# Kernel optimization log

Measured on AMD Instinct MI355X. Metric: run time of the kernel, lower is better.

Reference implementation:

```python
import jax, jax.numpy as jnp
import numpy as np

CHANNELS = 512
COND_DIM = 768
NUM_HEADS = 8
NUM_GROUPS = 32
EPS = 1e-5


def setup_inputs() -> dict:
    key = jax.random.key(0)
    ks = jax.random.split(key, 8)
    B, H, W, C, S = 8, 64, 64, CHANNELS, 256
    x = jax.random.normal(ks[0], (B, H, W, C), dtype=jnp.float32)
    cond_tokens = jax.random.normal(ks[1], (B, S, COND_DIM), dtype=jnp.float32)
    gn_scale = jnp.ones((C,), dtype=jnp.float32)
    gn_bias = jnp.zeros((C,), dtype=jnp.float32)
    Wq = jax.random.normal(ks[2], (C, CHANNELS), dtype=jnp.float32) * 0.02
    Wk = jax.random.normal(ks[3], (COND_DIM, CHANNELS), dtype=jnp.float32) * 0.02
    Wv = jax.random.normal(ks[4], (COND_DIM, CHANNELS), dtype=jnp.float32) * 0.02
    Wo = jax.random.normal(ks[5], (CHANNELS, CHANNELS), dtype=jnp.float32) * 0.02
    bo = jnp.zeros((CHANNELS,), dtype=jnp.float32)
    return {"x": x, "cond_tokens": cond_tokens, "gn_scale": gn_scale,
            "gn_bias": gn_bias, "Wq": Wq, "Wk": Wk, "Wv": Wv, "Wo": Wo, "bo": bo}


def group_norm(x, scale, bias):
    # x: (B,H,W,C); normalize over H,W and channels within each of NUM_GROUPS groups
    b, h, w, c = x.shape
    xg = x.reshape(b, h, w, NUM_GROUPS, c // NUM_GROUPS)
    mean = jnp.mean(xg, axis=(1, 2, 4), keepdims=True)
    var = jnp.var(xg, axis=(1, 2, 4), keepdims=True)
    xn = (xg - mean) * jax.lax.rsqrt(var + EPS)
    return xn.reshape(b, h, w, c) * scale + bias


def reference(x, cond_tokens, gn_scale, gn_bias, Wq, Wk, Wv, Wo, bo):
    b, h, w, c = x.shape
    head_dim = CHANNELS // NUM_HEADS
    x_seq = group_norm(x, gn_scale, gn_bias).reshape(b, h * w, c)
    # projections
    q = (x_seq @ Wq).reshape(b, -1, NUM_HEADS, head_dim).transpose(0, 2, 1, 3)
    k = (cond_tokens @ Wk).reshape(b, -1, NUM_HEADS, head_dim).transpose(0, 2, 1, 3)
    v = (cond_tokens @ Wv).reshape(b, -1, NUM_HEADS, head_dim).transpose(0, 2, 1, 3)
    scores = jnp.einsum('bhqd,bhkd->bhqk', q, k) / np.sqrt(head_dim).astype(np.float32)
    attn = jax.nn.softmax(scores, axis=-1)
    out = jnp.einsum('bhqk,bhkd->bhqd', attn, v)
    out = out.transpose(0, 2, 1, 3).reshape(b, h * w, CHANNELS)
    out = out @ Wo + bo
    return x + out.reshape(b, h, w, c)
```

## Files before the change

### kernel.cpp

```cpp
#include <hip/hip_runtime.h>
#include <hip/hip_bf16.h>

typedef unsigned short u16;
typedef unsigned int u32;
typedef __attribute__((ext_vector_type(8))) __bf16 bf16x8;
typedef __attribute__((ext_vector_type(4))) float f32x4;
typedef __attribute__((ext_vector_type(16))) float f32x16;
typedef __attribute__((ext_vector_type(4))) u32 u32x4;

#define DEVFN static __device__ __forceinline__

DEVFN float bf2f(u16 v) { union { u32 u; float f; } x; x.u = (u32)v << 16; return x.f; }
DEVFN u16 f2bf(float f) {
    union { float f; u32 u; } x; x.f = f;
    u32 r = x.u + 0x7fff + ((x.u >> 16) & 1);
    return (u16)(r >> 16);
}

union BF2 { struct { __bf16 lo, hi; } s; u32 w; };
DEVFN u32 pk2(float a, float b) { BF2 t; t.s.lo = (__bf16)a; t.s.hi = (__bf16)b; return t.w; }

DEVFN void gload_lds16(const u16* g, u16* l) {
    __builtin_amdgcn_global_load_lds((const __attribute__((address_space(1))) u32*)g,
                                     (__attribute__((address_space(3))) u32*)l, 16, 0, 0);
}

template<int OUTMODE, bool BIAS, bool RES, bool AFF>
__global__ __launch_bounds__(256)
void gemm_bt(const void* __restrict__ Av, const u16* __restrict__ B,
             const u16* __restrict__ B2,
             void* __restrict__ Cv, void* __restrict__ Cv2,
             const float* __restrict__ bias, const float* __restrict__ res,
             const float* __restrict__ cfA, const float* __restrict__ cfD,
             int K, int lda, int ldb, int ldc, float scale)
{
    __shared__ u16 smem[16384];
    const int tid = threadIdx.x;
    const int lane = tid & 63, wave = tid >> 6;
    const int wr = wave >> 1, wc = wave & 1;
    const u16* Bsel = (OUTMODE == 3 && blockIdx.z) ? B2 : B;
    const u16* Bb = Bsel + (long)blockIdx.y * 128 * ldb;
    const int ra = tid >> 2, ca = (tid & 3) * 8;
    const int foff = ((lane & 15) * 4 + (lane >> 4)) * 8;

    f32x4 acc[4][4];
#pragma unroll
    for (int i = 0; i < 4; ++i)
#pragma unroll
        for (int j = 0; j < 4; ++j) acc[i][j] = (f32x4){0.f, 0.f, 0.f, 0.f};

    const int nt = K >> 5;

    auto stageB = [&](int t, u16* bb) {
#pragma unroll
        for (int p = 0; p < 2; ++p)
            gload_lds16(Bb + (long)(p * 64 + ra) * ldb + t * 32 + ca,
                        bb + (p * 256 + tid) * 8);
    };
    const u16* Ab = (const u16*)Av + (long)blockIdx.x * 128 * lda;
    auto stageA = [&](int t, u16* ab) {
#pragma unroll
        for (int p = 0; p < 2; ++p)
            gload_lds16(Ab + (long)(p * 64 + ra) * lda + t * 32 + ca,
                        ab + (p * 256 + tid) * 8);
    };
    const float* xf = (const float*)Av;
    float4 xr[2][2], ar[2][2], dr[2][2];
    auto affLoad = [&](int t) {
#pragma unroll
        for (int p = 0; p < 2; ++p) {
            long m = (long)blockIdx.x * 128 + p * 64 + ra;
            int c = t * 32 + ca;
            const float* src = xf + m * lda + c;
            xr[p][0] = *(const float4*)(src);
            xr[p][1] = *(const float4*)(src + 4);
            int cb = (int)((m >> 12) << 9) + c;
            ar[p][0] = *(const float4*)(cfA + cb);
            ar[p][1] = *(const float4*)(cfA + cb + 4);
            dr[p][0] = *(const float4*)(cfD + cb);
            dr[p][1] = *(const float4*)(cfD + cb + 4);
        }
    };
    auto affWrite = [&](u16* ab) {
#pragma unroll
        for (int p = 0; p < 2; ++p) {
            u32x4 o;
            o[0] = pk2(xr[p][0].x * ar[p][0].x + dr[p][0].x,
                       xr[p][0].y * ar[p][0].y + dr[p][0].y);
            o[1] = pk2(xr[p][0].z * ar[p][0].z + dr[p][0].z,
                       xr[p][0].w * ar[p][0].w + dr[p][0].w);
            o[2] = pk2(xr[p][1].x * ar[p][1].x + dr[p][1].x,
                       xr[p][1].y * ar[p][1].y + dr[p][1].y);
            o[3] = pk2(xr[p][1].z * ar[p][1].z + dr[p][1].z,
                       xr[p][1].w * ar[p][1].w + dr[p][1].w);
            *(u32x4*)(ab + (p * 256 + tid) * 8) = o;
        }
    };

    stageB(0, smem + 4096);
    if constexpr (AFF) { affLoad(0); affWrite(smem); }
    else               stageA(0, smem);

    int cur = 0;
    for (int t = 0; t < nt; ++t) {
        asm volatile("s_waitcnt vmcnt(0)" ::: "memory");
        __syncthreads();
        const int nxt = cur ^ 1;
        u16* cA = smem + cur * 8192;
        u16* cB = smem + cur * 8192 + 4096;
        u16* nA = smem + nxt * 8192;
        u16* nB = smem + nxt * 8192 + 4096;
        const bool more = (t + 1 < nt);
        if (more) {
            stageB(t + 1, nB);
            if constexpr (AFF) affLoad(t + 1);
            else               stageA(t + 1, nA);
        }
        bf16x8 av[4], bv[4];
#pragma unroll
        for (int i = 0; i < 4; ++i) av[i] = *(const bf16x8*)(cA + (wr * 4 + i) * 512 + foff);
#pragma unroll
        for (int j = 0; j < 4; ++j) bv[j] = *(const bf16x8*)(cB + (wc * 4 + j) * 512 + foff);
        __builtin_amdgcn_s_setprio(1);
#pragma unroll
        for (int i = 0; i < 4; ++i)
#pragma unroll
            for (int j = 0; j < 4; ++j)
                acc[i][j] = __builtin_amdgcn_mfma_f32_16x16x32_bf16(av[i], bv[j], acc[i][j], 0, 0, 0);
        __builtin_amdgcn_s_setprio(0);
        if (more) { if constexpr (AFF) affWrite(nA); }
        cur = nxt;
    }

    const int m0 = blockIdx.x * 128 + wr * 64 + (lane >> 4) * 4;
    const int n0 = blockIdx.y * 128 + wc * 64 + (lane & 15);
    if constexpr (OUTMODE == 0) {
        u16* Cb = (u16*)Cv;
#pragma unroll
        for (int i = 0; i < 4; ++i)
#pragma unroll
            for (int j = 0; j < 4; ++j) {
                int n = n0 + j * 16;
#pragma unroll
                for (int r = 0; r < 4; ++r) {
                    int m = m0 + i * 16 + r;
                    Cb[(long)m * ldc + n] = f2bf(acc[i][j][r] * scale);
                }
            }
    } else if constexpr (OUTMODE == 1) {
        float* cl = (float*)smem;
        float* Co = (float*)Cv;
#pragma unroll
        for (int i = 0; i < 4; ++i) {
            __syncthreads();
#pragma unroll
            for (int j = 0; j < 4; ++j)
#pragma unroll
                for (int r = 0; r < 4; ++r) {
                    int rl = wr * 16 + (lane >> 4) * 4 + r;
                    int col = wc * 64 + j * 16 + (lane & 15);
                    cl[rl * 132 + col] = acc[i][j][r];
                }
            __syncthreads();
            int rl = tid >> 3;
            int c0 = (tid & 7) * 16;
            long m = (long)blockIdx.x * 128 + i * 16 + (rl & 15) + (rl >> 4) * 64;
            long n = (long)blockIdx.y * 128 + c0;
#pragma unroll
            for (int q = 0; q < 4; ++q) {
                float4 v = *(float4*)(cl + rl * 132 + c0 + q * 4);
                float4 o;
                o.x = v.x * scale; o.y = v.y * scale;
                o.z = v.z * scale; o.w = v.w * scale;
                if constexpr (BIAS) {
                    float4 b4 = *(const float4*)(bias + n + q * 4);
                    o.x += b4.x; o.y += b4.y; o.z += b4.z; o.w += b4.w;
                }
                if constexpr (RES) {
                    float4 r4 = *(const float4*)(res + m * ldc + n + q * 4);
                    o.x += r4.x; o.y += r4.y; o.z += r4.z; o.w += r4.w;
                }
                *(float4*)(Co + m * ldc + n + q * 4) = o;
            }
        }
    } else if constexpr (OUTMODE == 2) {
#pragma unroll
        for (int i = 0; i < 4; ++i) {
            int m = m0 + i * 16;
            int b = m >> 8, s = m & 255;
#pragma unroll
            for (int j = 0; j < 4; ++j) {
                int n = n0 + j * 16;
                int h = n >> 6, d = n & 63;
                ushort4 pk;
                pk.x = f2bf(acc[i][j][0]); pk.y = f2bf(acc[i][j][1]);
                pk.z = f2bf(acc[i][j][2]); pk.w = f2bf(acc[i][j][3]);
                *(ushort4*)((u16*)Cv + (((long)(b * 8 + h) * 64 + d) * 256 + s)) = pk;
            }
        }
    } else {
        if (blockIdx.z == 0) {
            u16* Cb = (u16*)Cv;
#pragma unroll
            for (int i = 0; i < 4; ++i)
#pragma unroll
                for (int j = 0; j < 4; ++j) {
                    int n = n0 + j * 16;
#pragma unroll
                    for (int r = 0; r < 4; ++r) {
                        int m = m0 + i * 16 + r;
                        Cb[(long)m * ldc + n] = f2bf(acc[i][j][r] * scale);
                    }
                }
        } else {
#pragma unroll
            for (int i = 0; i < 4; ++i) {
                int m = m0 + i * 16;
                int b = m >> 8, s = m & 255;
#pragma unroll
                for (int j = 0; j < 4; ++j) {
                    int n = n0 + j * 16;
                    int h = n >> 6, d = n & 63;
                    ushort4 pk;
                    pk.x = f2bf(acc[i][j][0]); pk.y = f2bf(acc[i][j][1]);
                    pk.z = f2bf(acc[i][j][2]); pk.w = f2bf(acc[i][j][3]);
                    *(ushort4*)((u16*)Cv2 + (((long)(b * 8 + h) * 64 + d) * 256 + s)) = pk;
                }
            }
        }
    }
}

union U8 { u32 w[4]; bf16x8 v; };

__global__ __launch_bounds__(512, 4)
void attn_fused(const u16* __restrict__ Q, const u16* __restrict__ K,
                const u16* __restrict__ Vt, u16* __restrict__ O)
{
    __shared__ u16 lds[40960];
    const int tid = threadIdx.x, lane = tid & 63, wave = tid >> 6;
    const int bh = blockIdx.y, b = bh >> 3, h = bh & 7;
    const int l31 = lane & 31, lh = lane >> 5;
    const long q0 = (long)b * 4096 + blockIdx.x * 256 + wave * 32;
    const bool hiHalf = (lh != 0);

    {
        const u16* Kb_ = K + (long)b * 256 * 512 + h * 64;
        const u16* Vb_ = Vt + (long)bh * 16384;
#pragma unroll
        for (int it = 0; it < 4; ++it) {
            int f = it * 8 + wave;
            int st = f >> 2, kc = f & 3;
            gload_lds16(Kb_ + (long)(st * 32 + l31) * 512 + kc * 16 + lh * 8,
                        lds + f * 512 + lane * 8);
            int dt = f >> 4, ks = f & 15;
            gload_lds16(Vb_ + (long)(dt * 32 + l31) * 256 + ks * 16 + lh * 8,
                        lds + 16384 + f * 512 + lane * 8);
        }
    }
    bf16x8 qf[4];
    {
        const u16* Qp = Q + (q0 + l31) * 512 + h * 64 + lh * 8;
#pragma unroll
        for (int kc = 0; kc < 4; ++kc) qf[kc] = *(const bf16x8*)(Qp + kc * 16);
    }
    asm volatile("s_waitcnt vmcnt(0)" ::: "memory");
    __syncthreads();

    f32x16 oacc[2];
#pragma unroll
    for (int dt = 0; dt < 2; ++dt)
#pragma unroll
        for (int r = 0; r < 16; ++r) oacc[dt][r] = 0.f;
    float m_run = -3e38f, sum_run = 0.f;

#pragma unroll
    for (int st = 0; st < 8; ++st) {
        f32x16 sc;
#pragma unroll
        for (int r = 0; r < 16; ++r) sc[r] = 0.f;
        __builtin_amdgcn_s_setprio(1);
#pragma unroll
        for (int kc = 0; kc < 4; ++kc) {
            bf16x8 af = *(const bf16x8*)(lds + (st * 4 + kc) * 512 + lane * 8);
            sc = __builtin_amdgcn_mfma_f32_32x32x16_bf16(af, qf[kc], sc, 0, 0, 0);
        }
        __builtin_amdgcn_s_setprio(0);
        float tm = sc[0];
#pragma unroll
        for (int r = 1; r < 16; ++r) tm = fmaxf(tm, sc[r]);
        tm = fmaxf(tm, __shfl_xor(tm, 32));
        if (!__all(tm <= m_run + 8.f)) {
            float mnew = fmaxf(m_run, tm);
            float fac = exp2f(m_run - mnew);
            m_run = mnew;
            sum_run *= fac;
#pragma unroll
            for (int dt = 0; dt < 2; ++dt)
#pragma unroll
                for (int r = 0; r < 16; ++r) oacc[dt][r] *= fac;
        }
#pragma unroll
        for (int r = 0; r < 16; ++r) {
            float e = exp2f(sc[r] - m_run);
            sc[r] = e; sum_run += e;
        }
        u32 c[8], x[8];
#pragma unroll
        for (int i = 0; i < 8; ++i) c[i] = pk2(sc[2 * i], sc[2 * i + 1]);
#pragma unroll
        for (int i = 0; i < 8; ++i) x[i] = (u32)__shfl_xor((int)c[i], 32);
        U8 p0, p1;
        p0.w[0] = hiHalf ? x[2] : c[0];  p0.w[1] = hiHalf ? x[3] : c[1];
        p0.w[2] = hiHalf ? c[2] : x[0];  p0.w[3] = hiHalf ? c[3] : x[1];
        p1.w[0] = hiHalf ? x[6] : c[4];  p1.w[1] = hiHalf ? x[7] : c[5];
        p1.w[2] = hiHalf ? c[6] : x[4];  p1.w[3] = hiHalf ? c[7] : x[5];
        __builtin_amdgcn_s_setprio(1);
#pragma unroll
        for (int dt = 0; dt < 2; ++dt) {
            bf16x8 v0 = *(const bf16x8*)(lds + 16384 + (dt * 16 + st * 2) * 512 + lane * 8);
            bf16x8 v1 = *(const bf16x8*)(lds + 16384 + (dt * 16 + st * 2 + 1) * 512 + lane * 8);
            oacc[dt] = __builtin_amdgcn_mfma_f32_32x32x16_bf16(v0, p0.v, oacc[dt], 0, 0, 0);
            oacc[dt] = __builtin_amdgcn_mfma_f32_32x32x16_bf16(v1, p1.v, oacc[dt], 0, 0, 0);
        }
        __builtin_amdgcn_s_setprio(0);
    }

    sum_run += __shfl_xor(sum_run, 32);
    float inv = 1.f / sum_run;

    u16* ow = lds + 32768 + (wave & 3) * 2048;
    const int shift = wave >> 2;
#pragma unroll
    for (int s_ = 0; s_ < 2; ++s_) {
        if (s_ == 1) __syncthreads();
        if (shift == s_) {
            const int q = l31;
#pragma unroll
            for (int dt = 0; dt < 2; ++dt)
#pragma unroll
                for (int rq = 0; rq < 4; ++rq) {
                    int d = dt * 32 + rq * 8 + 4 * lh;
                    u32 w0 = pk2(oacc[dt][rq * 4 + 0] * inv, oacc[dt][rq * 4 + 1] * inv);
                    u32 w1 = pk2(oacc[dt][rq * 4 + 2] * inv, oacc[dt][rq * 4 + 3] * inv);
                    int byte = q * 128 + ((d * 2) ^ ((q & 7) << 4));
                    *(u32*)((char*)ow + byte) = w0;
                    *(u32*)((char*)ow + byte + 4) = w1;
                }
#pragma unroll
            for (int i = 0; i < 4; ++i) {
                int qq = (lane >> 3) + i * 8;
                int byte = qq * 128 + (((lane & 7) * 16) ^ ((qq & 7) << 4));
                bf16x8 val = *(const bf16x8*)((char*)ow + byte);
                *(bf16x8*)(O + (q0 + qq) * 512 + h * 64 + (lane & 7) * 8) = val;
            }
        }
    }
}

__global__ __launch_bounds__(256)
void gn_part(const float* __restrict__ x, float* __restrict__ part)
{
    const int b = blockIdx.x, ch = blockIdx.y;
    const float* base = x + ((long)b * 4096 + ch * 64) * 512;
    const int t = threadIdx.x;
    const int c4 = t & 127, r0 = t >> 7;
    float sum = 0.f, sq = 0.f;
    for (int rr = r0; rr < 64; rr += 2) {
        float4 v = *(const float4*)(base + (long)rr * 512 + c4 * 4);
        sum += v.x + v.y + v.z + v.w;
        sq  += v.x * v.x + v.y * v.y + v.z * v.z + v.w * v.w;
    }
    __shared__ float s0[128], s1[128];
    if (t >= 128) { s0[c4] = sum; s1[c4] = sq; }
    __syncthreads();
    if (t < 128) {
        sum += s0[c4]; sq += s1[c4];
        sum += __shfl_down(sum, 2); sum += __shfl_down(sum, 1);
        sq  += __shfl_down(sq, 2);  sq  += __shfl_down(sq, 1);
        if ((t & 3) == 0) {
            int g = t >> 2;
            float* pp = part + (long)(b * 64 + ch) * 64;
            pp[g] = sum; pp[32 + g] = sq;
        }
    }
}

__global__ __launch_bounds__(256)
void gn_coef(const float* __restrict__ part, const float* __restrict__ gscale,
             const float* __restrict__ gbias, float* __restrict__ coefA,
             float* __restrict__ coefD)
{
    const int t = threadIdx.x;
    const int b = t >> 5, g = t & 31;
    float S = 0.f, Q = 0.f;
    for (int ch = 0; ch < 64; ++ch) {
        const float* pp = part + (long)(b * 64 + ch) * 64;
        S += pp[g]; Q += pp[32 + g];
    }
    float mean = S * (1.f / 65536.f);
    float var = Q * (1.f / 65536.f) - mean * mean;
    float rstd = rsqrtf(var + 1e-5f);
#pragma unroll
    for (int cc = 0; cc < 16; ++cc) {
        int c = g * 16 + cc;
        float a = gscale[c] * rstd;
        coefA[b * 512 + c] = a;
        coefD[b * 512 + c] = gbias[c] - mean * a;
    }
}

__global__ __launch_bounds__(256)
void conv_bf16(const float* __restrict__ in, u16* __restrict__ out)
{
    long e = ((long)blockIdx.x * 256 + threadIdx.x) * 8;
    float4 v0 = *(const float4*)(in + e);
    float4 v1 = *(const float4*)(in + e + 4);
    float f[8] = { v0.x, v0.y, v0.z, v0.w, v1.x, v1.y, v1.z, v1.w };
    u32x4 o;
#pragma unroll
    for (int q = 0; q < 4; ++q)
        o[q] = (u32)f2bf(f[q * 2]) | ((u32)f2bf(f[q * 2 + 1]) << 16);
    *(u32x4*)(out + e) = o;
}

__global__ __launch_bounds__(256)
void transpose_all(const float* __restrict__ Wq, const float* __restrict__ Wk,
                   const float* __restrict__ Wv, const float* __restrict__ Wo,
                   u16* __restrict__ WqT, u16* __restrict__ WkT,
                   u16* __restrict__ WvT, u16* __restrict__ WoT)
{
    __shared__ u16 t[32][33];
    const int z = blockIdx.z;
    const float* in = (z == 0) ? Wq : (z == 1) ? Wk : (z == 2) ? Wv : Wo;
    u16* out = (z == 0) ? WqT : (z == 1) ? WkT : (z == 2) ? WvT : WoT;
    const int R = (z == 1 || z == 2) ? 768 : 512, C = 512;
    const int r0 = blockIdx.y * 32, c0 = blockIdx.x * 32;
    if (r0 >= R) return;
    int tx = threadIdx.x & 31, ty = threadIdx.x >> 5;
    for (int i = ty; i < 32; i += 8) t[i][tx] = f2bf(in[(long)(r0 + i) * C + c0 + tx]);
    __syncthreads();
    for (int i = ty; i < 32; i += 8) out[(long)(c0 + i) * R + r0 + tx] = t[tx][i];
}

extern "C" void kernel_launch(void* const* d_in, const int* in_sizes, int n_in,
                              void* d_out, int out_size, void* d_ws, size_t ws_size,
                              hipStream_t stream)
{
    const float* x    = (const float*)d_in[0];
    const float* cond = (const float*)d_in[1];
    const float* gsc  = (const float*)d_in[2];
    const float* gbi  = (const float*)d_in[3];
    const float* Wq   = (const float*)d_in[4];
    const float* Wk   = (const float*)d_in[5];
    const float* Wv   = (const float*)d_in[6];
    const float* Wo   = (const float*)d_in[7];
    const float* bo   = (const float*)d_in[8];

    char* ws = (char*)d_ws;
    size_t off = 0;
    auto alloc = [&](size_t bytes) -> void* {
        void* p = ws + off; off += (bytes + 255) & ~(size_t)255; return p;
    };
    u16* WqT    = (u16*)alloc(512 * 512 * 2);
    u16* WkT    = (u16*)alloc(512 * 768 * 2);
    u16* WvT    = (u16*)alloc(512 * 768 * 2);
    u16* WoT    = (u16*)alloc(512 * 512 * 2);
    float* cfA  = (float*)alloc(8 * 512 * 4);
    float* cfD  = (float*)alloc(8 * 512 * 4);
    float* part = (float*)alloc(8 * 64 * 64 * 4);
    u16* condb  = (u16*)alloc(2048l * 768 * 2);
    u16* Ob     = (u16*)alloc(33554432);
    u16* Qb     = (u16*)alloc(33554432);
    u16* Kb     = (u16*)alloc(2048l * 512 * 2);
    u16* Vt     = (u16*)alloc(2097152);

    transpose_all<<<dim3(16, 24, 4), 256, 0, stream>>>(Wq, Wk, Wv, Wo, WqT, WkT, WvT, WoT);
    conv_bf16<<<768, 256, 0, stream>>>(cond, condb);

    gn_part<<<dim3(8, 64), 256, 0, stream>>>(x, part);
    gn_coef<<<1, 256, 0, stream>>>(part, gsc, gbi, cfA, cfD);

    gemm_bt<0, false, false, true><<<dim3(256, 4), 256, 0, stream>>>(
        x, WqT, nullptr, Qb, nullptr, nullptr, nullptr, cfA, cfD,
        512, 512, 512, 512, 0.18033688011112042f);
    gemm_bt<3, false, false, false><<<dim3(16, 4, 2), 256, 0, stream>>>(
        condb, WkT, WvT, Kb, Vt, nullptr, nullptr, nullptr, nullptr,
        768, 768, 768, 512, 1.f);

    attn_fused<<<dim3(16, 64), 512, 0, stream>>>(Qb, Kb, Vt, Ob);

    gemm_bt<1, true, true, false><<<dim3(256, 4), 256, 0, stream>>>(
        Ob, WoT, nullptr, d_out, nullptr, bo, x, nullptr, nullptr,
        512, 512, 512, 512, 1.f);
}
```

Before: 176.9 us.

## Fold GroupNorm affine into per-batch Wq and cache bf16 copy of x

The GroupNorm scale is folded into a per-batch, pre-scaled and transposed copy of Wq. The shift becomes a per-batch bias on Q, computed by a small matvec kernel. The stats pass now also writes a bf16 copy of x, so the Q GEMM can stream A through async global-to-LDS loads instead of loading fp32 and applying the affine in registers. The output GEMM reads its residual from that bf16 copy instead of fp32 x, which cuts memory traffic but lowers residual precision and adds 8 per-batch weight matrices plus extra small kernels.

```diff
diff --git a/kernel.cpp b/kernel.cpp
--- a/kernel.cpp
+++ b/kernel.cpp
@@ -8,6 +8,8 @@
 typedef __attribute__((ext_vector_type(16))) float f32x16;
 typedef __attribute__((ext_vector_type(4))) u32 u32x4;
 
+#define SCL 0.18033688011112042f
+
 #define DEVFN static __device__ __forceinline__
 
 DEVFN float bf2f(u16 v) { union { u32 u; float f; } x; x.u = (u32)v << 16; return x.f; }
@@ -25,13 +27,12 @@
                                      (__attribute__((address_space(3))) u32*)l, 16, 0, 0);
 }
 
-template<int OUTMODE, bool BIAS, bool RES, bool AFF>
-__global__ __launch_bounds__(256)
-void gemm_bt(const void* __restrict__ Av, const u16* __restrict__ B,
+template<int OUTMODE, bool BIAS, bool RES, bool PERB, bool RESBF>
+__global__ __launch_bounds__(256)
+void gemm_bt(const u16* __restrict__ A, const u16* __restrict__ B,
              const u16* __restrict__ B2,
              void* __restrict__ Cv, void* __restrict__ Cv2,
-             const float* __restrict__ bias, const float* __restrict__ res,
-             const float* __restrict__ cfA, const float* __restrict__ cfD,
+             const float* __restrict__ bias, const void* __restrict__ res,
              int K, int lda, int ldb, int ldc, float scale)
 {
     __shared__ u16 smem[16384];
@@ -39,7 +40,9 @@
     const int lane = tid & 63, wave = tid >> 6;
     const int wr = wave >> 1, wc = wave & 1;
     const u16* Bsel = (OUTMODE == 3 && blockIdx.z) ? B2 : B;
+    if constexpr (PERB) Bsel += (long)(blockIdx.x >> 5) * 262144;
     const u16* Bb = Bsel + (long)blockIdx.y * 128 * ldb;
+    const u16* Ab = A + (long)blockIdx.x * 128 * lda;
     const int ra = tid >> 2, ca = (tid & 3) * 8;
     const int foff = ((lane & 15) * 4 + (lane >> 4)) * 8;
 
@@ -50,57 +53,18 @@
         for (int j = 0; j < 4; ++j) acc[i][j] = (f32x4){0.f, 0.f, 0.f, 0.f};
 
     const int nt = K >> 5;
-
-    auto stageB = [&](int t, u16* bb) {
+    auto stage = [&](int t, u16* buf) {
+#pragma unroll
+        for (int p = 0; p < 2; ++p)
+            gload_lds16(Ab + (long)(p * 64 + ra) * lda + t * 32 + ca,
+                        buf + (p * 256 + tid) * 8);
 #pragma unroll
         for (int p = 0; p < 2; ++p)
             gload_lds16(Bb + (long)(p * 64 + ra) * ldb + t * 32 + ca,
-                        bb + (p * 256 + tid) * 8);
+                        buf + 4096 + (p * 256 + tid) * 8);
     };
-    const u16* Ab = (const u16*)Av + (long)blockIdx.x * 128 * lda;
-    auto stageA = [&](int t, u16* ab) {
-#pragma unroll
-        for (int p = 0; p < 2; ++p)
-            gload_lds16(Ab + (long)(p * 64 + ra) * lda + t * 32 + ca,
-                        ab + (p * 256 + tid) * 8);
-    };
-    const float* xf = (const float*)Av;
-    float4 xr[2][2], ar[2][2], dr[2][2];
-    auto affLoad = [&](int t) {
-#pragma unroll
-        for (int p = 0; p < 2; ++p) {
-            long m = (long)blockIdx.x * 128 + p * 64 + ra;
-            int c = t * 32 + ca;
-            const float* src = xf + m * lda + c;
-            xr[p][0] = *(const float4*)(src);
-            xr[p][1] = *(const float4*)(src + 4);
-            int cb = (int)((m >> 12) << 9) + c;
-            ar[p][0] = *(const float4*)(cfA + cb);
-            ar[p][1] = *(const float4*)(cfA + cb + 4);
-            dr[p][0] = *(const float4*)(cfD + cb);
-            dr[p][1] = *(const float4*)(cfD + cb + 4);
-        }
-    };
-    auto affWrite = [&](u16* ab) {
-#pragma unroll
-        for (int p = 0; p < 2; ++p) {
-            u32x4 o;
-            o[0] = pk2(xr[p][0].x * ar[p][0].x + dr[p][0].x,
-                       xr[p][0].y * ar[p][0].y + dr[p][0].y);
-            o[1] = pk2(xr[p][0].z * ar[p][0].z + dr[p][0].z,
-                       xr[p][0].w * ar[p][0].w + dr[p][0].w);
-            o[2] = pk2(xr[p][1].x * ar[p][1].x + dr[p][1].x,
-                       xr[p][1].y * ar[p][1].y + dr[p][1].y);
-            o[3] = pk2(xr[p][1].z * ar[p][1].z + dr[p][1].z,
-                       xr[p][1].w * ar[p][1].w + dr[p][1].w);
-            *(u32x4*)(ab + (p * 256 + tid) * 8) = o;
-        }
-    };
-
-    stageB(0, smem + 4096);
-    if constexpr (AFF) { affLoad(0); affWrite(smem); }
-    else               stageA(0, smem);
-
+
+    stage(0, smem);
     int cur = 0;
     for (int t = 0; t < nt; ++t) {
         asm volatile("s_waitcnt vmcnt(0)" ::: "memory");
@@ -108,14 +72,7 @@
         const int nxt = cur ^ 1;
         u16* cA = smem + cur * 8192;
         u16* cB = smem + cur * 8192 + 4096;
-        u16* nA = smem + nxt * 8192;
-        u16* nB = smem + nxt * 8192 + 4096;
-        const bool more = (t + 1 < nt);
-        if (more) {
-            stageB(t + 1, nB);
-            if constexpr (AFF) affLoad(t + 1);
-            else               stageA(t + 1, nA);
-        }
+        if (t + 1 < nt) stage(t + 1, smem + nxt * 8192);
         bf16x8 av[4], bv[4];
 #pragma unroll
         for (int i = 0; i < 4; ++i) av[i] = *(const bf16x8*)(cA + (wr * 4 + i) * 512 + foff);
@@ -128,7 +85,6 @@
             for (int j = 0; j < 4; ++j)
                 acc[i][j] = __builtin_amdgcn_mfma_f32_16x16x32_bf16(av[i], bv[j], acc[i][j], 0, 0, 0);
         __builtin_amdgcn_s_setprio(0);
-        if (more) { if constexpr (AFF) affWrite(nA); }
         cur = nxt;
     }
 
@@ -136,15 +92,18 @@
     const int n0 = blockIdx.y * 128 + wc * 64 + (lane & 15);
     if constexpr (OUTMODE == 0) {
         u16* Cb = (u16*)Cv;
+        const float* bp = bias;
+        if constexpr (PERB && BIAS) bp += (blockIdx.x >> 5) * 512;
 #pragma unroll
         for (int i = 0; i < 4; ++i)
 #pragma unroll
             for (int j = 0; j < 4; ++j) {
                 int n = n0 + j * 16;
+                float bv_ = BIAS ? bp[n] : 0.f;
 #pragma unroll
                 for (int r = 0; r < 4; ++r) {
                     int m = m0 + i * 16 + r;
-                    Cb[(long)m * ldc + n] = f2bf(acc[i][j][r] * scale);
+                    Cb[(long)m * ldc + n] = f2bf(acc[i][j][r] * scale + bv_);
                 }
             }
     } else if constexpr (OUTMODE == 1) {
@@ -177,25 +136,16 @@
                     o.x += b4.x; o.y += b4.y; o.z += b4.z; o.w += b4.w;
                 }
                 if constexpr (RES) {
-                    float4 r4 = *(const float4*)(res + m * ldc + n + q * 4);
-                    o.x += r4.x; o.y += r4.y; o.z += r4.z; o.w += r4.w;
+                    if constexpr (RESBF) {
+                        ushort4 r4 = *(const ushort4*)((const u16*)res + m * ldc + n + q * 4);
+                        o.x += bf2f(r4.x); o.y += bf2f(r4.y);
+                        o.z += bf2f(r4.z); o.w += bf2f(r4.w);
+                    } else {
+                        float4 r4 = *(const float4*)((const float*)res + m * ldc + n + q * 4);
+                        o.x += r4.x; o.y += r4.y; o.z += r4.z; o.w += r4.w;
+                    }
                 }
                 *(float4*)(Co + m * ldc + n + q * 4) = o;
-            }
-        }
-    } else if constexpr (OUTMODE == 2) {
-#pragma unroll
-        for (int i = 0; i < 4; ++i) {
-            int m = m0 + i * 16;
-            int b = m >> 8, s = m & 255;
-#pragma unroll
-            for (int j = 0; j < 4; ++j) {
-                int n = n0 + j * 16;
-                int h = n >> 6, d = n & 63;
-                ushort4 pk;
-                pk.x = f2bf(acc[i][j][0]); pk.y = f2bf(acc[i][j][1]);
-                pk.z = f2bf(acc[i][j][2]); pk.w = f2bf(acc[i][j][3]);
-                *(ushort4*)((u16*)Cv + (((long)(b * 8 + h) * 64 + d) * 256 + s)) = pk;
             }
         }
     } else {
@@ -359,17 +309,23 @@
 }
 
 __global__ __launch_bounds__(256)
-void gn_part(const float* __restrict__ x, float* __restrict__ part)
+void gn_part(const float* __restrict__ x, float* __restrict__ part,
+             u16* __restrict__ xb)
 {
     const int b = blockIdx.x, ch = blockIdx.y;
-    const float* base = x + ((long)b * 4096 + ch * 64) * 512;
+    const long base = ((long)b * 4096 + ch * 64) * 512;
+    const float* bx = x + base;
+    u16* bo = xb + base;
     const int t = threadIdx.x;
     const int c4 = t & 127, r0 = t >> 7;
     float sum = 0.f, sq = 0.f;
     for (int rr = r0; rr < 64; rr += 2) {
-        float4 v = *(const float4*)(base + (long)rr * 512 + c4 * 4);
+        float4 v = *(const float4*)(bx + (long)rr * 512 + c4 * 4);
         sum += v.x + v.y + v.z + v.w;
         sq  += v.x * v.x + v.y * v.y + v.z * v.z + v.w * v.w;
+        uint2 w;
+        w.x = pk2(v.x, v.y); w.y = pk2(v.z, v.w);
+        *(uint2*)(bo + (long)rr * 512 + c4 * 4) = w;
     }
     __shared__ float s0[128], s1[128];
     if (t >= 128) { s0[c4] = sum; s1[c4] = sq; }
@@ -411,6 +367,36 @@
 }
 
 __global__ __launch_bounds__(256)
+void scale_wq(const float* __restrict__ Wq, const float* __restrict__ cfA,
+              u16* __restrict__ WqS)
+{
+    __shared__ u16 t[32][33];
+    const int b = blockIdx.z;
+    const int r0 = blockIdx.y * 32, c0 = blockIdx.x * 32;
+    int tx = threadIdx.x & 31, ty = threadIdx.x >> 5;
+    for (int i = ty; i < 32; i += 8)
+        t[i][tx] = f2bf(Wq[(long)(r0 + i) * 512 + c0 + tx] * cfA[b * 512 + r0 + i] * SCL);
+    __syncthreads();
+    for (int i = ty; i < 32; i += 8)
+        WqS[(long)b * 262144 + (long)(c0 + i) * 512 + r0 + tx] = t[tx][i];
+}
+
+__global__ __launch_bounds__(256)
+void dq_bias(const float* __restrict__ Wq, const float* __restrict__ cfD,
+             float* __restrict__ dq)
+{
+    const int b = blockIdx.x, t = threadIdx.x;
+    float a0 = 0.f, a1 = 0.f;
+    for (int c = 0; c < 512; ++c) {
+        float d = cfD[b * 512 + c];
+        a0 += d * Wq[(long)c * 512 + t];
+        a1 += d * Wq[(long)c * 512 + t + 256];
+    }
+    dq[b * 512 + t] = a0 * SCL;
+    dq[b * 512 + t + 256] = a1 * SCL;
+}
+
+__global__ __launch_bounds__(256)
 void conv_bf16(const float* __restrict__ in, u16* __restrict__ out)
 {
     long e = ((long)blockIdx.x * 256 + threadIdx.x) * 8;
@@ -425,16 +411,16 @@
 }
 
 __global__ __launch_bounds__(256)
-void transpose_all(const float* __restrict__ Wq, const float* __restrict__ Wk,
-                   const float* __restrict__ Wv, const float* __restrict__ Wo,
-                   u16* __restrict__ WqT, u16* __restrict__ WkT,
-                   u16* __restrict__ WvT, u16* __restrict__ WoT)
+void transpose_all(const float* __restrict__ Wk, const float* __restrict__ Wv,
+                   const float* __restrict__ Wo,
+                   u16* __restrict__ WkT, u16* __restrict__ WvT,
+                   u16* __restrict__ WoT)
 {
     __shared__ u16 t[32][33];
     const int z = blockIdx.z;
-    const float* in = (z == 0) ? Wq : (z == 1) ? Wk : (z == 2) ? Wv : Wo;
-    u16* out = (z == 0) ? WqT : (z == 1) ? WkT : (z == 2) ? WvT : WoT;
-    const int R = (z == 1 || z == 2) ? 768 : 512, C = 512;
+    const float* in = (z == 0) ? Wk : (z == 1) ? Wv : Wo;
+    u16* out = (z == 0) ? WkT : (z == 1) ? WvT : WoT;
+    const int R = (z < 2) ? 768 : 512, C = 512;
     const int r0 = blockIdx.y * 32, c0 = blockIdx.x * 32;
     if (r0 >= R) return;
     int tx = threadIdx.x & 31, ty = threadIdx.x >> 5;
@@ -462,35 +448,37 @@
     auto alloc = [&](size_t bytes) -> void* {
         void* p = ws + off; off += (bytes + 255) & ~(size_t)255; return p;
     };
-    u16* WqT    = (u16*)alloc(512 * 512 * 2);
     u16* WkT    = (u16*)alloc(512 * 768 * 2);
     u16* WvT    = (u16*)alloc(512 * 768 * 2);
     u16* WoT    = (u16*)alloc(512 * 512 * 2);
+    u16* WqS    = (u16*)alloc(8l * 512 * 512 * 2);
     float* cfA  = (float*)alloc(8 * 512 * 4);
     float* cfD  = (float*)alloc(8 * 512 * 4);
+    float* dq   = (float*)alloc(8 * 512 * 4);
     float* part = (float*)alloc(8 * 64 * 64 * 4);
     u16* condb  = (u16*)alloc(2048l * 768 * 2);
+    u16* xb     = (u16*)alloc(33554432);
     u16* Ob     = (u16*)alloc(33554432);
     u16* Qb     = (u16*)alloc(33554432);
     u16* Kb     = (u16*)alloc(2048l * 512 * 2);
     u16* Vt     = (u16*)alloc(2097152);
 
-    transpose_all<<<dim3(16, 24, 4), 256, 0, stream>>>(Wq, Wk, Wv, Wo, WqT, WkT, WvT, WoT);
+    transpose_all<<<dim3(16, 24, 3), 256, 0, stream>>>(Wk, Wv, Wo, WkT, WvT, WoT);
     conv_bf16<<<768, 256, 0, stream>>>(cond, condb);
 
-    gn_part<<<dim3(8, 64), 256, 0, stream>>>(x, part);
+    gn_part<<<dim3(8, 64), 256, 0, stream>>>(x, part, xb);
     gn_coef<<<1, 256, 0, stream>>>(part, gsc, gbi, cfA, cfD);
-
-    gemm_bt<0, false, false, true><<<dim3(256, 4), 256, 0, stream>>>(
-        x, WqT, nullptr, Qb, nullptr, nullptr, nullptr, cfA, cfD,
-        512, 512, 512, 512, 0.18033688011112042f);
-    gemm_bt<3, false, false, false><<<dim3(16, 4, 2), 256, 0, stream>>>(
-        condb, WkT, WvT, Kb, Vt, nullptr, nullptr, nullptr, nullptr,
-        768, 768, 768, 512, 1.f);
+    scale_wq<<<dim3(16, 16, 8), 256, 0, stream>>>(Wq, cfA, WqS);
+    dq_bias<<<8, 256, 0, stream>>>(Wq, cfD, dq);
+
+    gemm_bt<3, false, false, false, false><<<dim3(16, 4, 2), 256, 0, stream>>>(
+        condb, WkT, WvT, Kb, Vt, nullptr, nullptr, 768, 768, 768, 512, 1.f);
+
+    gemm_bt<0, true, false, true, false><<<dim3(256, 4), 256, 0, stream>>>(
+        xb, WqS, nullptr, Qb, nullptr, dq, nullptr, 512, 512, 512, 512, 1.f);
 
     attn_fused<<<dim3(16, 64), 512, 0, stream>>>(Qb, Kb, Vt, Ob);
 
-    gemm_bt<1, true, true, false><<<dim3(256, 4), 256, 0, stream>>>(
-        Ob, WoT, nullptr, d_out, nullptr, bo, x, nullptr, nullptr,
-        512, 512, 512, 512, 1.f);
-}
+    gemm_bt<1, true, true, false, true><<<dim3(256, 4), 256, 0, stream>>>(
+        Ob, WoT, nullptr, d_out, nullptr, bo, xb, 512, 512, 512, 512, 1.f);
+}
```

After: 197.4 us. 11.6% more time.
